# Kernel optimization log

Measured on AMD Instinct MI355X. Metric: run time of the kernel, lower is better.

The kernel has to match this reference:

```python
import jax, jax.numpy as jnp
import numpy as np
import math

E = 1024      # embed_dim
H = 16        # num_heads
HD = E // H   # head_dim
NBITS = 8


def fake_quant(x, n_bits=NBITS):
    """Symmetric per-tensor fake quantize with STE (clamp/round/dequant)."""
    qmax = 2.0 ** (n_bits - 1) - 1.0
    qmin = -(2.0 ** (n_bits - 1))
    scale = jnp.maximum(jnp.max(jnp.abs(x)) / qmax, 1e-8)
    xq = jnp.round(jnp.clip(x / scale, qmin, qmax)) * scale
    return x + jax.lax.stop_gradient(xq - x)


def setup_inputs() -> dict:
    key = jax.random.key(0)
    ks = jax.random.split(key, 7)
    L, B = 2048, 2
    query = jax.random.normal(ks[0], (L, B, E), dtype=jnp.float32)
    k_in = jax.random.normal(ks[1], (L, B, E), dtype=jnp.float32)
    v_in = jax.random.normal(ks[2], (L, B, E), dtype=jnp.float32)
    in_w = jax.random.normal(ks[3], (3 * E, E), dtype=jnp.float32) * (1.0 / math.sqrt(E))
    in_b = jax.random.normal(ks[4], (3 * E,), dtype=jnp.float32) * 0.01
    out_w = jax.random.normal(ks[5], (E, E), dtype=jnp.float32) * (1.0 / math.sqrt(E))
    out_b = jax.random.normal(ks[6], (E,), dtype=jnp.float32) * 0.01
    return {"query": query, "key": k_in, "value": v_in,
            "in_w": in_w, "in_b": in_b, "out_w": out_w, "out_b": out_b}


def reference(query, key, value, in_w, in_b, out_w, out_b):
    # NOTE: the original module ignores `key`/`value` (pure self-attention on query),
    # and its attn / softmax fake-quant lines are dead statements (results discarded).
    L, B, _ = query.shape
    Wi = fake_quant(in_w)
    Wo = fake_quant(out_w)
    # input projection: [L,B,3E]
    X = jnp.einsum('lbe,fe->lbf', query, Wi) + in_b
    X = fake_quant(X)
    Q, K, V = jnp.split(X, 3, axis=-1)  # each [L,B,E]
    # [L, B*H, HD] -> [B*H, L, HD]
    q = Q.reshape(L, B * H, HD).transpose(1, 0, 2)
    k = K.reshape(L, B * H, HD).transpose(1, 0, 2)
    v = V.reshape(L, B * H, HD).transpose(1, 0, 2)
    q = q / math.sqrt(HD)
    q = fake_quant(q)
    attn = jnp.einsum('bqd,bkd->bqk', q, k)          # [B*H, L, L]
    attn = jax.nn.softmax(attn, axis=-1)
    heads = jnp.einsum('bqk,bkd->bqd', attn, v)      # [B*H, L, HD]
    heads = fake_quant(heads)
    # [B*H, L, HD] -> [L, B*H, HD] -> [L*B, E]
    heads_r = heads.transpose(1, 0, 2).reshape(L * B, E)
    y = heads_r @ Wo.T + out_b
    y = y.reshape(L, B, E)
    return fake_quant(y)
```

## Files before the change

kernel.cpp:

```cpp
#include <hip/hip_runtime.h>
#include <math.h>

#define L_SEQ 2048
#define BATCH 2
#define EMB 1024
#define NH 16
#define HDIM 64
#define F3 3072
#define NROWS 4096

typedef __bf16 bf16_t;
typedef short s16x8 __attribute__((ext_vector_type(8)));
typedef float f32x4 __attribute__((ext_vector_type(4)));

#define MFMA16(a, b, c) __builtin_amdgcn_mfma_f32_16x16x32_bf16(a, b, c, 0, 0, 0)


__device__ __forceinline__ float u2f(unsigned u) { return __uint_as_float(u); }

__device__ __forceinline__ void gload16(const bf16_t* g, bf16_t* lds) {
  __builtin_amdgcn_global_load_lds((const __attribute__((address_space(1))) void*)g,
                                   (__attribute__((address_space(3))) void*)lds, 16, 0, 0);
}

__device__ __forceinline__ void blockmax_commit(float m, unsigned* slot) {
  #pragma unroll
  for (int o = 1; o < 64; o <<= 1) m = fmaxf(m, __shfl_xor(m, o));
  __shared__ float sm_[4];
  if ((threadIdx.x & 63) == 0) sm_[threadIdx.x >> 6] = m;
  __syncthreads();
  if (threadIdx.x == 0) {
    float mm = fmaxf(fmaxf(sm_[0], sm_[1]), fmaxf(sm_[2], sm_[3]));
    atomicMax(slot, __float_as_uint(mm));
  }
}

__global__ __launch_bounds__(256) void wabsmax_k(const float* __restrict__ wi,
                                                 const float* __restrict__ wo,
                                                 unsigned* __restrict__ slots) {
  float m0 = 0.0f, m1 = 0.0f;
  const int n0 = F3 * EMB / 4, n1 = EMB * EMB / 4;
  for (int i = blockIdx.x * blockDim.x + threadIdx.x; i < n0; i += gridDim.x * blockDim.x) {
    float4 v = ((const float4*)wi)[i];
    m0 = fmaxf(m0, fmaxf(fmaxf(fabsf(v.x), fabsf(v.y)), fmaxf(fabsf(v.z), fabsf(v.w))));
  }
  for (int i = blockIdx.x * blockDim.x + threadIdx.x; i < n1; i += gridDim.x * blockDim.x) {
    float4 v = ((const float4*)wo)[i];
    m1 = fmaxf(m1, fmaxf(fmaxf(fabsf(v.x), fabsf(v.y)), fmaxf(fabsf(v.z), fabsf(v.w))));
  }
  blockmax_commit(m0, slots + 0);
  blockmax_commit(m1, slots + 1);
}

__global__ __launch_bounds__(256) void prep_k(const float* __restrict__ wi,
                                              const float* __restrict__ wo,
                                              const float* __restrict__ query,
                                              bf16_t* __restrict__ Wi_int,
                                              bf16_t* __restrict__ Wo_int,
                                              bf16_t* __restrict__ q_hi,
                                              bf16_t* __restrict__ q_lo,
                                              const unsigned* __restrict__ slots) {
  float s0 = fmaxf(u2f(slots[0]) / 127.0f, 1e-8f);
  float s1 = fmaxf(u2f(slots[1]) / 127.0f, 1e-8f);
  const int n0 = F3 * EMB / 4, n1 = EMB * EMB / 4, n2 = NROWS * EMB / 4;
  for (int i = blockIdx.x * blockDim.x + threadIdx.x; i < n0; i += gridDim.x * blockDim.x) {
    float4 v = ((const float4*)wi)[i];
    bf16_t o[4];
    o[0] = (bf16_t)rintf(fminf(fmaxf(v.x / s0, -128.0f), 127.0f));
    o[1] = (bf16_t)rintf(fminf(fmaxf(v.y / s0, -128.0f), 127.0f));
    o[2] = (bf16_t)rintf(fminf(fmaxf(v.z / s0, -128.0f), 127.0f));
    o[3] = (bf16_t)rintf(fminf(fmaxf(v.w / s0, -128.0f), 127.0f));
    *(uint2*)&Wi_int[(size_t)i * 4] = *(uint2*)o;
  }
  for (int i = blockIdx.x * blockDim.x + threadIdx.x; i < n1; i += gridDim.x * blockDim.x) {
    float4 v = ((const float4*)wo)[i];
    bf16_t o[4];
    o[0] = (bf16_t)rintf(fminf(fmaxf(v.x / s1, -128.0f), 127.0f));
    o[1] = (bf16_t)rintf(fminf(fmaxf(v.y / s1, -128.0f), 127.0f));
    o[2] = (bf16_t)rintf(fminf(fmaxf(v.z / s1, -128.0f), 127.0f));
    o[3] = (bf16_t)rintf(fminf(fmaxf(v.w / s1, -128.0f), 127.0f));
    *(uint2*)&Wo_int[(size_t)i * 4] = *(uint2*)o;
  }
  for (int i = blockIdx.x * blockDim.x + threadIdx.x; i < n2; i += gridDim.x * blockDim.x) {
    float4 v = ((const float4*)query)[i];
    bf16_t h[4], l[4];
    float vv[4] = {v.x, v.y, v.z, v.w};
    #pragma unroll
    for (int j = 0; j < 4; ++j) {
      h[j] = (bf16_t)vv[j];
      l[j] = (bf16_t)(vv[j] - (float)h[j]);
    }
    *(uint2*)&q_hi[(size_t)i * 4] = *(uint2*)h;
    *(uint2*)&q_lo[(size_t)i * 4] = *(uint2*)l;
  }
}

__global__ __launch_bounds__(256) void quantX_k(const float* __restrict__ x,
                                                bf16_t* __restrict__ y,
                                                unsigned* __restrict__ slots) {
  float s = fmaxf(u2f(slots[2]) / 127.0f, 1e-8f);
  float qm = 0.0f;
  const int n8 = NROWS * 256;
  for (int i = blockIdx.x * blockDim.x + threadIdx.x; i < n8; i += gridDim.x * blockDim.x) {
    int row = i >> 8, ch = i & 255;
    const float* px = x + (size_t)row * F3 + ch * 8;
    float4 v0 = *(const float4*)px;
    float4 v1 = *(const float4*)(px + 4);
    float vv[8] = {v0.x, v0.y, v0.z, v0.w, v1.x, v1.y, v1.z, v1.w};
    bf16_t o[8];
    float lm = 0.0f;
    #pragma unroll
    for (int j = 0; j < 8; ++j) {
      float q = rintf(fminf(fmaxf(vv[j] / s, -128.0f), 127.0f));
      o[j] = (bf16_t)q;
      lm = fmaxf(lm, fabsf(q));
    }
    if (ch < 128) qm = fmaxf(qm, lm);
    *(uint4*)&y[(size_t)row * F3 + ch * 8] = *(uint4*)o;
  }
  blockmax_commit(qm, slots + 3);
}

__global__ __launch_bounds__(256) void quant_k(float* __restrict__ x, int n4,
                                               const unsigned* __restrict__ slots, int sloti) {
  float s = fmaxf(u2f(slots[sloti]) / 127.0f, 1e-8f);
  float4* x4 = (float4*)x;
  for (int i = blockIdx.x * blockDim.x + threadIdx.x; i < n4; i += gridDim.x * blockDim.x) {
    float4 v = x4[i];
    v.x = rintf(fminf(fmaxf(v.x / s, -128.0f), 127.0f)) * s;
    v.y = rintf(fminf(fmaxf(v.y / s, -128.0f), 127.0f)) * s;
    v.z = rintf(fminf(fmaxf(v.z / s, -128.0f), 127.0f)) * s;
    v.w = rintf(fminf(fmaxf(v.w / s, -128.0f), 127.0f)) * s;
    x4[i] = v;
  }
}

__global__ __launch_bounds__(256) void quantf_k(const float* __restrict__ x,
                                                bf16_t* __restrict__ y, int n4,
                                                const unsigned* __restrict__ slots, int sloti) {
  float s = fmaxf(u2f(slots[sloti]) / 127.0f, 1e-8f);
  const float4* x4 = (const float4*)x;
  for (int i = blockIdx.x * blockDim.x + threadIdx.x; i < n4; i += gridDim.x * blockDim.x) {
    float4 v = x4[i];
    bf16_t o[4];
    o[0] = (bf16_t)rintf(fminf(fmaxf(v.x / s, -128.0f), 127.0f));
    o[1] = (bf16_t)rintf(fminf(fmaxf(v.y / s, -128.0f), 127.0f));
    o[2] = (bf16_t)rintf(fminf(fmaxf(v.z / s, -128.0f), 127.0f));
    o[3] = (bf16_t)rintf(fminf(fmaxf(v.w / s, -128.0f), 127.0f));
    *(uint2*)&y[(size_t)i * 4] = *(uint2*)o;
  }
}

__global__ __launch_bounds__(256) void vtrans_k(const float* __restrict__ X,
                                                bf16_t* __restrict__ Vt,
                                                const unsigned* __restrict__ slots) {
  float s = fmaxf(u2f(slots[2]) / 127.0f, 1e-8f);
  __shared__ __align__(16) bf16_t tile[64][72];
  int tt = blockIdx.x, bh = blockIdx.y;
  int b = bh >> 4, h = bh & 15;
  int t = threadIdx.x;
  #pragma unroll
  for (int i = 0; i < 2; ++i) {
    int s_ = t + i * 256;
    int tok = s_ >> 3, seg = s_ & 7;
    const float* px = X + ((size_t)(tt * 64 + tok) * BATCH + b) * F3 + 2 * EMB + h * HDIM + seg * 8;
    float4 v0 = *(const float4*)px;
    float4 v1 = *(const float4*)(px + 4);
    float vv[8] = {v0.x, v0.y, v0.z, v0.w, v1.x, v1.y, v1.z, v1.w};
    bf16_t o[8];
    #pragma unroll
    for (int j = 0; j < 8; ++j)
      o[j] = (bf16_t)rintf(fminf(fmaxf(vv[j] / s, -128.0f), 127.0f));
    int segs = seg ^ (tok >> 3);
    *(uint4*)&tile[tok][segs * 8] = *(uint4*)o;
  }
  __syncthreads();
  #pragma unroll
  for (int i = 0; i < 2; ++i) {
    int s_ = t + i * 256;
    int d = s_ >> 3, tseg = s_ & 7;
    bf16_t o[8];
    #pragma unroll
    for (int e = 0; e < 8; ++e) {
      int tok = tseg * 8 + e;
      o[e] = tile[tok][(((d >> 3) ^ (tok >> 3)) << 3) | (d & 7)];
    }
    *(uint4*)&Vt[((size_t)bh * HDIM + d) * L_SEQ + tt * 64 + tseg * 8] = *(uint4*)o;
  }
}

template <int NPARTS>
__global__ __launch_bounds__(256) void gemm_bt_mfma_k(const bf16_t* __restrict__ A0,
                                                      const bf16_t* __restrict__ A1,
                                                      const bf16_t* __restrict__ Bm,
                                                      const float* __restrict__ bias,
                                                      float* __restrict__ C,
                                                      int M, int N, int K,
                                                      unsigned* __restrict__ slots,
                                                      int sa, int sb, int smax) {
  __shared__ __align__(16) bf16_t sbuf[2][NPARTS + 1][128][32];
  int t = threadIdx.x;
  int w = t >> 6, l = t & 63, c15 = l & 15, g = l >> 4;
  int wr = w >> 1, wc = w & 1;
  int nx = gridDim.x;
  int fid = blockIdx.y * nx + blockIdx.x;
  int qq = (nx * gridDim.y) >> 3;
  int swz = (fid & 7) * qq + (fid >> 3);
  int bm = (swz / nx) * 128, bn = (swz % nx) * 128;
  f32x4 acc[4][4] = {};

  auto stage = [&](int bf, int k0) {
    #pragma unroll
    for (int i = 0; i < 2; ++i) {
      int c = i * 256 + t;
      int row = c >> 2, sg = c & 3;
      int wb = (i * 256 + w * 64) * 8;
      gload16(&A0[(size_t)(bm + row) * K + k0 + sg * 8], &sbuf[bf][0][0][0] + wb);
      if (NPARTS == 2)
        gload16(&A1[(size_t)(bm + row) * K + k0 + sg * 8], &sbuf[bf][1][0][0] + wb);
      gload16(&Bm[(size_t)(bn + row) * K + k0 + sg * 8], &sbuf[bf][NPARTS][0][0] + wb);
    }
  };

  stage(0, 0);
  __syncthreads();
  const int nk = K / 32;
  for (int kt = 0; kt < nk; ++kt) {
    int cur = kt & 1;
    if (kt + 1 < nk) stage(cur ^ 1, (kt + 1) * 32);
    s16x8 af[NPARTS][4], bf_[4];
    #pragma unroll
    for (int rt = 0; rt < 4; ++rt) {
      af[0][rt] = *(const s16x8*)&sbuf[cur][0][wr * 64 + rt * 16 + c15][g * 8];
      if (NPARTS == 2) af[1][rt] = *(const s16x8*)&sbuf[cur][1][wr * 64 + rt * 16 + c15][g * 8];
    }
    #pragma unroll
    for (int ct = 0; ct < 4; ++ct)
      bf_[ct] = *(const s16x8*)&sbuf[cur][NPARTS][wc * 64 + ct * 16 + c15][g * 8];
    __builtin_amdgcn_s_setprio(1);
    #pragma unroll
    for (int rt = 0; rt < 4; ++rt)
      #pragma unroll
      for (int ct = 0; ct < 4; ++ct) {
        acc[rt][ct] = MFMA16(af[0][rt], bf_[ct], acc[rt][ct]);
        if (NPARTS == 2) acc[rt][ct] = MFMA16(af[1][rt], bf_[ct], acc[rt][ct]);
      }
    __builtin_amdgcn_s_setprio(0);
    __syncthreads();
  }

  float s = 1.0f;
  if (sa >= 0) s *= fmaxf(u2f(slots[sa]) / 127.0f, 1e-8f);
  if (sb >= 0) s *= fmaxf(u2f(slots[sb]) / 127.0f, 1e-8f);
  float vmax = 0.0f;
  #pragma unroll
  for (int rt = 0; rt < 4; ++rt)
    #pragma unroll
    for (int r = 0; r < 4; ++r) {
      int row = bm + wr * 64 + rt * 16 + 4 * g + r;
      #pragma unroll
      for (int ct = 0; ct < 4; ++ct) {
        int col = bn + wc * 64 + ct * 16 + c15;
        float o = acc[rt][ct][r] * s + bias[col];
        vmax = fmaxf(vmax, fabsf(o));
        C[(size_t)row * N + col] = o;
      }
    }
  if (smax >= 0) blockmax_commit(vmax, slots + smax);
}

__global__ __launch_bounds__(256) void attn_mfma_k(const bf16_t* __restrict__ X,
                                                   const bf16_t* __restrict__ Vt,
                                                   float* __restrict__ heads,
                                                   unsigned* __restrict__ slots) {
  int qb = blockIdx.x, bh = blockIdx.y;
  int b = bh >> 4, h = bh & 15;
  int t = threadIdx.x;
  int w = t >> 6, l = t & 63, c15 = l & 15, g = l >> 4;

  float s_x = fmaxf(u2f(slots[2]) / 127.0f, 1e-8f);
  float s_q = fmaxf((u2f(slots[3]) * s_x) * 0.125f / 127.0f, 1e-8f);
  const float LOG2E = 1.4426950408889634f;
  float qsl2 = s_q * s_x * LOG2E;

  __shared__ __align__(16) union SmKV {
    struct { bf16_t K[2][64][64]; bf16_t V[2][64][64]; } kv;
    float Ot[4][16][69];
  } sm;

  int qrow = qb * 64 + w * 16 + c15;
  const bf16_t* qbase = X + ((size_t)qrow * BATCH + b) * F3 + h * HDIM;
  s16x8 qf0, qf1;
  {
    bf16_t qt[8];
    #pragma unroll
    for (int half = 0; half < 2; ++half) {
      *(uint4*)qt = *(const uint4*)(qbase + half * 32 + g * 8);
      #pragma unroll
      for (int j = 0; j < 8; ++j) {
        float q = ((float)qt[j] * s_x) * 0.125f;
        qt[j] = (bf16_t)rintf(fminf(fmaxf(q / s_q, -128.0f), 127.0f));
      }
      if (half == 0) qf0 = *(s16x8*)qt; else qf1 = *(s16x8*)qt;
    }
  }

  const size_t tokstride = (size_t)BATCH * F3;
  const bf16_t* kbase = X + (size_t)b * F3 + EMB + h * HDIM;
  const bf16_t* vbase = Vt + (size_t)bh * HDIM * L_SEQ;

  auto stage = [&](int buf, int kt) {
    #pragma unroll
    for (int i = 0; i < 2; ++i) {
      int c = i * 256 + t;
      int a = c >> 3, blk = c & 7;
      int kap = (a & 0x20) | ((a & 0x10) >> 2) | ((a & 0x0C) << 1) | (a & 3);
      gload16(kbase + (size_t)(kt * 64 + kap) * tokstride + (blk ^ (a & 7)) * 8,
              &sm.kv.K[buf][0][0] + (i * 256 + w * 64) * 8);
    }
    #pragma unroll
    for (int i = 0; i < 2; ++i) {
      int c = i * 256 + t;
      int d = c >> 3, blk = c & 7;
      gload16(vbase + (size_t)d * L_SEQ + kt * 64 + (blk ^ (d & 7)) * 8,
              &sm.kv.V[buf][0][0] + (i * 256 + w * 64) * 8);
    }
  };

  f32x4 acc_o[4] = {};
  float m_prev = -INFINITY, lsum = 0.0f;
  int sw = c15 & 7;

  stage(0, 0);
  __syncthreads();

  const int NT = L_SEQ / 64;
  int cur = 0;
  for (int kt = 0; kt < NT; ++kt) {
    if (kt + 1 < NT) stage(cur ^ 1, kt + 1);

    f32x4 accs[4] = {};
    __builtin_amdgcn_s_setprio(1);
    #pragma unroll
    for (int ct = 0; ct < 4; ++ct) {
      const bf16_t* krow = &sm.kv.K[cur][ct * 16 + c15][0];
      s16x8 kf0 = *(const s16x8*)(krow + (g ^ sw) * 8);
      s16x8 kf1 = *(const s16x8*)(krow + ((g | 4) ^ sw) * 8);
      accs[ct] = MFMA16(kf0, qf0, accs[ct]);
      accs[ct] = MFMA16(kf1, qf1, accs[ct]);
    }
    __builtin_amdgcn_s_setprio(0);

    float pm = accs[0][0];
    #pragma unroll
    for (int ct = 0; ct < 4; ++ct)
      #pragma unroll
      for (int r = 0; r < 4; ++r) pm = fmaxf(pm, accs[ct][r]);
    pm = fmaxf(pm, __shfl_xor(pm, 16));
    pm = fmaxf(pm, __shfl_xor(pm, 32));
    float mnew = fmaxf(m_prev, pm);
    float f_ = __builtin_amdgcn_exp2f((m_prev - mnew) * qsl2);
    float mq = mnew * qsl2;
    float ps = 0.0f;
    bf16_t hh[2][8], ll[2][8];
    #pragma unroll
    for (int ct = 0; ct < 4; ++ct) {
      float p[4];
      #pragma unroll
      for (int r = 0; r < 4; ++r) p[r] = __builtin_amdgcn_exp2f(fmaf(accs[ct][r], qsl2, -mq));
      ps += (p[0] + p[1]) + (p[2] + p[3]);
      #pragma unroll
      for (int r = 0; r < 4; ++r) {
        bf16_t hi = (bf16_t)p[r];
        hh[ct >> 1][(ct & 1) * 4 + r] = hi;
        ll[ct >> 1][(ct & 1) * 4 + r] = (bf16_t)(p[r] - (float)hi);
      }
    }
    lsum = lsum * f_ + ps;
    m_prev = mnew;

    if (!__all(f_ == 1.0f)) {
      #pragma unroll
      for (int dt = 0; dt < 4; ++dt)
        #pragma unroll
        for (int r = 0; r < 4; ++r) acc_o[dt][r] *= f_;
    }

    s16x8 pfh0 = *(s16x8*)hh[0], pfh1 = *(s16x8*)hh[1];
    s16x8 pfl0 = *(s16x8*)ll[0], pfl1 = *(s16x8*)ll[1];
    __builtin_amdgcn_s_setprio(1);
    #pragma unroll
    for (int dt = 0; dt < 4; ++dt) {
      const bf16_t* vrow = &sm.kv.V[cur][dt * 16 + c15][0];
      s16x8 vf0 = *(const s16x8*)(vrow + (g ^ sw) * 8);
      s16x8 vf1 = *(const s16x8*)(vrow + ((g | 4) ^ sw) * 8);
      acc_o[dt] = MFMA16(vf0, pfh0, acc_o[dt]);
      acc_o[dt] = MFMA16(vf1, pfh1, acc_o[dt]);
      acc_o[dt] = MFMA16(vf0, pfl0, acc_o[dt]);
      acc_o[dt] = MFMA16(vf1, pfl1, acc_o[dt]);
    }
    __builtin_amdgcn_s_setprio(0);

    __syncthreads();
    cur ^= 1;
  }

  lsum += __shfl_xor(lsum, 16);
  lsum += __shfl_xor(lsum, 32);
  float inv = s_x / lsum;

  float hm = 0.0f;
  #pragma unroll
  for (int dt = 0; dt < 4; ++dt)
    #pragma unroll
    for (int r = 0; r < 4; ++r) {
      float o = acc_o[dt][r] * inv;
      hm = fmaxf(hm, fabsf(o));
      sm.Ot[w][c15][dt * 16 + 4 * g + r] = o;
    }
  int ql = l >> 2, cs = l & 3;
  #pragma unroll
  for (int j = 0; j < 4; ++j) {
    int cch = cs + 4 * j;
    float4 v = *(const float4*)&sm.Ot[w][ql][cch * 4];
    int row = qb * 64 + w * 16 + ql;
    *(float4*)&heads[((size_t)row * BATCH + b) * EMB + h * HDIM + cch * 4] = v;
  }
  blockmax_commit(hm, slots + 4);
}

extern "C" void kernel_launch(void* const* d_in, const int* in_sizes, int n_in,
                              void* d_out, int out_size, void* d_ws, size_t ws_size,
                              hipStream_t stream) {
  (void)in_sizes; (void)n_in; (void)out_size; (void)ws_size;
  const float* query = (const float*)d_in[0];
  const float* in_w  = (const float*)d_in[3];
  const float* in_b  = (const float*)d_in[4];
  const float* out_w = (const float*)d_in[5];
  const float* out_b = (const float*)d_in[6];
  float* out = (float*)d_out;

  unsigned* slots = (unsigned*)d_ws;
  char* p = (char*)d_ws + 256;
  bf16_t* q_hi   = (bf16_t*)p;                  p += (size_t)NROWS * EMB * 2;
  bf16_t* q_lo   = (bf16_t*)p;                  p += (size_t)NROWS * EMB * 2;
  bf16_t* Wi_int = (bf16_t*)p;                  p += (size_t)F3 * EMB * 2;
  bf16_t* Wo_int = (bf16_t*)p;                  p += (size_t)EMB * EMB * 2;
  float*  X_f32  = (float*)p;                   p += (size_t)NROWS * F3 * 4;
  bf16_t* X_int  = (bf16_t*)p;
  bf16_t* Vt     = q_hi;
  bf16_t* heads_int = (bf16_t*)X_f32;
  float*  heads_f32 = out;

  hipMemsetAsync(d_ws, 0, 256, stream);

  dim3 b256(256);
  wabsmax_k<<<768, b256, 0, stream>>>(in_w, out_w, slots);
  prep_k<<<1024, b256, 0, stream>>>(in_w, out_w, query, Wi_int, Wo_int, q_hi, q_lo, slots);

  gemm_bt_mfma_k<2><<<dim3(F3 / 128, NROWS / 128), b256, 0, stream>>>(
      q_hi, q_lo, Wi_int, in_b, X_f32, NROWS, F3, EMB, slots, -1, 0, 2);

  quantX_k<<<2048, b256, 0, stream>>>(X_f32, X_int, slots);

  vtrans_k<<<dim3(L_SEQ / 64, BATCH * NH), b256, 0, stream>>>(X_f32, Vt, slots);

  attn_mfma_k<<<dim3(L_SEQ / 64, BATCH * NH), b256, 0, stream>>>(X_int, Vt, heads_f32, slots);

  quantf_k<<<1024, b256, 0, stream>>>(heads_f32, heads_int, NROWS * EMB / 4, slots, 4);

  gemm_bt_mfma_k<1><<<dim3(EMB / 128, NROWS / 128), b256, 0, stream>>>(
      heads_int, nullptr, Wo_int, out_b, out, NROWS, EMB, EMB, slots, 4, 1, 5);

  quant_k<<<1024, b256, 0, stream>>>(out, NROWS * EMB / 4, slots, 5);
}
```

Measured before the change: 247.7 us.

## Process two query tiles per warp in attention to reuse K/V fragments

```diff
diff --git a/kernel.cpp b/kernel.cpp
--- a/kernel.cpp
+++ b/kernel.cpp
@@ -8,6 +8,7 @@
 #define HDIM 64
 #define F3 3072
 #define NROWS 4096
+#define QBLK 128
 
 typedef __bf16 bf16_t;
 typedef short s16x8 __attribute__((ext_vector_type(8)));
@@ -273,7 +274,7 @@
                                                    const bf16_t* __restrict__ Vt,
                                                    float* __restrict__ heads,
                                                    unsigned* __restrict__ slots) {
-  int qb = blockIdx.x, bh = blockIdx.y;
+  int bh = blockIdx.x, qb = blockIdx.y;
   int b = bh >> 4, h = bh & 15;
   int t = threadIdx.x;
   int w = t >> 6, l = t & 63, c15 = l & 15, g = l >> 4;
@@ -288,10 +289,11 @@
     float Ot[4][16][69];
   } sm;
 
-  int qrow = qb * 64 + w * 16 + c15;
-  const bf16_t* qbase = X + ((size_t)qrow * BATCH + b) * F3 + h * HDIM;
-  s16x8 qf0, qf1;
-  {
+  s16x8 qf0[2], qf1[2];
+  #pragma unroll
+  for (int tile = 0; tile < 2; ++tile) {
+    int qtok = qb * QBLK + w * 32 + tile * 16 + c15;
+    const bf16_t* qbase = X + ((size_t)qtok * BATCH + b) * F3 + h * HDIM;
     bf16_t qt[8];
     #pragma unroll
     for (int half = 0; half < 2; ++half) {
@@ -301,7 +303,7 @@
         float q = ((float)qt[j] * s_x) * 0.125f;
         qt[j] = (bf16_t)rintf(fminf(fmaxf(q / s_q, -128.0f), 127.0f));
       }
-      if (half == 0) qf0 = *(s16x8*)qt; else qf1 = *(s16x8*)qt;
+      if (half == 0) qf0[tile] = *(s16x8*)qt; else qf1[tile] = *(s16x8*)qt;
     }
   }
 
@@ -327,8 +329,9 @@
     }
   };
 
-  f32x4 acc_o[4] = {};
-  float m_prev = -INFINITY, lsum = 0.0f;
+  f32x4 acc_o[2][4] = {};
+  float m_prev[2] = {-INFINITY, -INFINITY};
+  float lsum[2] = {0.0f, 0.0f};
   int sw = c15 & 7;
 
   stage(0, 0);
@@ -339,65 +342,74 @@
   for (int kt = 0; kt < NT; ++kt) {
     if (kt + 1 < NT) stage(cur ^ 1, kt + 1);
 
-    f32x4 accs[4] = {};
+    f32x4 accs[2][4] = {};
     __builtin_amdgcn_s_setprio(1);
     #pragma unroll
     for (int ct = 0; ct < 4; ++ct) {
       const bf16_t* krow = &sm.kv.K[cur][ct * 16 + c15][0];
       s16x8 kf0 = *(const s16x8*)(krow + (g ^ sw) * 8);
       s16x8 kf1 = *(const s16x8*)(krow + ((g | 4) ^ sw) * 8);
-      accs[ct] = MFMA16(kf0, qf0, accs[ct]);
-      accs[ct] = MFMA16(kf1, qf1, accs[ct]);
+      accs[0][ct] = MFMA16(kf0, qf0[0], accs[0][ct]);
+      accs[0][ct] = MFMA16(kf1, qf1[0], accs[0][ct]);
+      accs[1][ct] = MFMA16(kf0, qf0[1], accs[1][ct]);
+      accs[1][ct] = MFMA16(kf1, qf1[1], accs[1][ct]);
     }
     __builtin_amdgcn_s_setprio(0);
 
-    float pm = accs[0][0];
-    #pragma unroll
-    for (int ct = 0; ct < 4; ++ct)
-      #pragma unroll
-      for (int r = 0; r < 4; ++r) pm = fmaxf(pm, accs[ct][r]);
-    pm = fmaxf(pm, __shfl_xor(pm, 16));
-    pm = fmaxf(pm, __shfl_xor(pm, 32));
-    float mnew = fmaxf(m_prev, pm);
-    float f_ = __builtin_amdgcn_exp2f((m_prev - mnew) * qsl2);
-    float mq = mnew * qsl2;
-    float ps = 0.0f;
-    bf16_t hh[2][8], ll[2][8];
-    #pragma unroll
-    for (int ct = 0; ct < 4; ++ct) {
-      float p[4];
-      #pragma unroll
-      for (int r = 0; r < 4; ++r) p[r] = __builtin_amdgcn_exp2f(fmaf(accs[ct][r], qsl2, -mq));
-      ps += (p[0] + p[1]) + (p[2] + p[3]);
-      #pragma unroll
-      for (int r = 0; r < 4; ++r) {
-        bf16_t hi = (bf16_t)p[r];
-        hh[ct >> 1][(ct & 1) * 4 + r] = hi;
-        ll[ct >> 1][(ct & 1) * 4 + r] = (bf16_t)(p[r] - (float)hi);
-      }
-    }
-    lsum = lsum * f_ + ps;
-    m_prev = mnew;
-
-    if (!__all(f_ == 1.0f)) {
-      #pragma unroll
-      for (int dt = 0; dt < 4; ++dt)
+    s16x8 pfh0[2], pfh1[2], pfl0[2], pfl1[2];
+    #pragma unroll
+    for (int tile = 0; tile < 2; ++tile) {
+      float pm = accs[tile][0][0];
+      #pragma unroll
+      for (int ct = 0; ct < 4; ++ct)
         #pragma unroll
-        for (int r = 0; r < 4; ++r) acc_o[dt][r] *= f_;
-    }
-
-    s16x8 pfh0 = *(s16x8*)hh[0], pfh1 = *(s16x8*)hh[1];
-    s16x8 pfl0 = *(s16x8*)ll[0], pfl1 = *(s16x8*)ll[1];
+        for (int r = 0; r < 4; ++r) pm = fmaxf(pm, accs[tile][ct][r]);
+      pm = fmaxf(pm, __shfl_xor(pm, 16));
+      pm = fmaxf(pm, __shfl_xor(pm, 32));
+      float mnew = fmaxf(m_prev[tile], pm);
+      float f_ = __builtin_amdgcn_exp2f((m_prev[tile] - mnew) * qsl2);
+      float mq = mnew * qsl2;
+      float ps = 0.0f;
+      bf16_t hh[2][8], ll[2][8];
+      #pragma unroll
+      for (int ct = 0; ct < 4; ++ct) {
+        float p[4];
+        #pragma unroll
+        for (int r = 0; r < 4; ++r)
+          p[r] = __builtin_amdgcn_exp2f(fmaf(accs[tile][ct][r], qsl2, -mq));
+        ps += (p[0] + p[1]) + (p[2] + p[3]);
+        #pragma unroll
+        for (int r = 0; r < 4; ++r) {
+          bf16_t hi = (bf16_t)p[r];
+          hh[ct >> 1][(ct & 1) * 4 + r] = hi;
+          ll[ct >> 1][(ct & 1) * 4 + r] = (bf16_t)(p[r] - (float)hi);
+        }
+      }
+      lsum[tile] = lsum[tile] * f_ + ps;
+      m_prev[tile] = mnew;
+      if (!__all(f_ == 1.0f)) {
+        #pragma unroll
+        for (int dt = 0; dt < 4; ++dt)
+          #pragma unroll
+          for (int r = 0; r < 4; ++r) acc_o[tile][dt][r] *= f_;
+      }
+      pfh0[tile] = *(s16x8*)hh[0]; pfh1[tile] = *(s16x8*)hh[1];
+      pfl0[tile] = *(s16x8*)ll[0]; pfl1[tile] = *(s16x8*)ll[1];
+    }
+
     __builtin_amdgcn_s_setprio(1);
     #pragma unroll
     for (int dt = 0; dt < 4; ++dt) {
       const bf16_t* vrow = &sm.kv.V[cur][dt * 16 + c15][0];
       s16x8 vf0 = *(const s16x8*)(vrow + (g ^ sw) * 8);
       s16x8 vf1 = *(const s16x8*)(vrow + ((g | 4) ^ sw) * 8);
-      acc_o[dt] = MFMA16(vf0, pfh0, acc_o[dt]);
-      acc_o[dt] = MFMA16(vf1, pfh1, acc_o[dt]);
-      acc_o[dt] = MFMA16(vf0, pfl0, acc_o[dt]);
-      acc_o[dt] = MFMA16(vf1, pfl1, acc_o[dt]);
+      #pragma unroll
+      for (int tile = 0; tile < 2; ++tile) {
+        acc_o[tile][dt] = MFMA16(vf0, pfh0[tile], acc_o[tile][dt]);
+        acc_o[tile][dt] = MFMA16(vf1, pfh1[tile], acc_o[tile][dt]);
+        acc_o[tile][dt] = MFMA16(vf0, pfl0[tile], acc_o[tile][dt]);
+        acc_o[tile][dt] = MFMA16(vf1, pfl1[tile], acc_o[tile][dt]);
+      }
     }
     __builtin_amdgcn_s_setprio(0);
 
@@ -405,26 +417,29 @@
     cur ^= 1;
   }
 
-  lsum += __shfl_xor(lsum, 16);
-  lsum += __shfl_xor(lsum, 32);
-  float inv = s_x / lsum;
-
   float hm = 0.0f;
-  #pragma unroll
-  for (int dt = 0; dt < 4; ++dt)
-    #pragma unroll
-    for (int r = 0; r < 4; ++r) {
-      float o = acc_o[dt][r] * inv;
-      hm = fmaxf(hm, fabsf(o));
-      sm.Ot[w][c15][dt * 16 + 4 * g + r] = o;
-    }
   int ql = l >> 2, cs = l & 3;
   #pragma unroll
-  for (int j = 0; j < 4; ++j) {
-    int cch = cs + 4 * j;
-    float4 v = *(const float4*)&sm.Ot[w][ql][cch * 4];
-    int row = qb * 64 + w * 16 + ql;
-    *(float4*)&heads[((size_t)row * BATCH + b) * EMB + h * HDIM + cch * 4] = v;
+  for (int tile = 0; tile < 2; ++tile) {
+    float l2 = lsum[tile];
+    l2 += __shfl_xor(l2, 16);
+    l2 += __shfl_xor(l2, 32);
+    float inv = s_x / l2;
+    #pragma unroll
+    for (int dt = 0; dt < 4; ++dt)
+      #pragma unroll
+      for (int r = 0; r < 4; ++r) {
+        float o = acc_o[tile][dt][r] * inv;
+        hm = fmaxf(hm, fabsf(o));
+        sm.Ot[w][c15][dt * 16 + 4 * g + r] = o;
+      }
+    #pragma unroll
+    for (int j = 0; j < 4; ++j) {
+      int cch = cs + 4 * j;
+      float4 v = *(const float4*)&sm.Ot[w][ql][cch * 4];
+      int tok = qb * QBLK + w * 32 + tile * 16 + ql;
+      *(float4*)&heads[((size_t)tok * BATCH + b) * EMB + h * HDIM + cch * 4] = v;
+    }
   }
   blockmax_commit(hm, slots + 4);
 }
@@ -465,7 +480,7 @@
 
   vtrans_k<<<dim3(L_SEQ / 64, BATCH * NH), b256, 0, stream>>>(X_f32, Vt, slots);
 
-  attn_mfma_k<<<dim3(L_SEQ / 64, BATCH * NH), b256, 0, stream>>>(X_int, Vt, heads_f32, slots);
+  attn_mfma_k<<<dim3(BATCH * NH, L_SEQ / QBLK), b256, 0, stream>>>(X_int, Vt, heads_f32, slots);
 
   quantf_k<<<1024, b256, 0, stream>>>(heads_f32, heads_int, NROWS * EMB / 4, slots, 4);
 
```

Result: no change. 245.2 us (-1.0%).
